# Kernel optimization log

Hardware: AMD Instinct MI355X
Metric: run time of the kernel (lower is better)

Reference implementation:

```python
import jax, jax.numpy as jnp
import numpy as np

N, T, E = 50000, 12, 800000
IN_DIM, SP_DIM, TP_DIM = 128, 128, 128


def setup_inputs() -> dict:
    key = jax.random.key(0)
    ks = jax.random.split(key, 9)
    h = jax.random.normal(ks[0], (N, T, IN_DIM), dtype=jnp.float32)
    src = jax.random.randint(ks[1], (E,), 0, N, dtype=jnp.int32)
    dst = jax.random.randint(ks[2], (E,), 0, N, dtype=jnp.int32)
    s = 1.0 / np.sqrt(IN_DIM).astype(np.float32)
    # GraphConv layer weights (xavier-ish) and zero biases, layer1: in->sp, layer2: sp->sp
    Wg1 = jax.random.normal(ks[3], (IN_DIM, SP_DIM), dtype=jnp.float32) * s
    bg1 = jnp.zeros((SP_DIM,), jnp.float32)
    Wg2 = jax.random.normal(ks[4], (SP_DIM, SP_DIM), dtype=jnp.float32) * s
    bg2 = jnp.zeros((SP_DIM,), jnp.float32)
    # LSTM params, torch layout: [4H, in]/[4H, H], gate order i,f,g,o
    t = 1.0 / np.sqrt(TP_DIM).astype(np.float32)
    w_ih = jax.random.uniform(ks[5], (4 * TP_DIM, IN_DIM), jnp.float32, -t, t)
    w_hh = jax.random.uniform(ks[6], (4 * TP_DIM, TP_DIM), jnp.float32, -t, t)
    b_ih = jax.random.uniform(ks[7], (4 * TP_DIM,), jnp.float32, -t, t)
    b_hh = jax.random.uniform(ks[8], (4 * TP_DIM,), jnp.float32, -t, t)
    return dict(h=h, src=src, dst=dst, Wg1=Wg1, bg1=bg1, Wg2=Wg2, bg2=bg2,
                w_ih=w_ih, w_hh=w_hh, b_ih=b_ih, b_hh=b_hh)


def _graph_conv(x, src, dst, norm_src, norm_dst, W, b):
    # DGL GraphConv norm='both': D_out^{-1/2} on source feats, sum-aggregate to dst,
    # D_in^{-1/2} on result, then dense weight + bias.
    x = x * norm_src                                  # [N, D]
    m = jax.ops.segment_sum(x[src], dst, num_segments=N)  # SpMM: [N, D]
    m = m * norm_dst
    return m @ W + b


def reference(h, src, dst, Wg1, bg1, Wg2, bg2, w_ih, w_hh, b_ih, b_hh):
    ones_e = jnp.ones((E,), jnp.float32)
    out_deg = jnp.maximum(jax.ops.segment_sum(ones_e, src, num_segments=N), 1.0)
    in_deg = jnp.maximum(jax.ops.segment_sum(ones_e, dst, num_segments=N), 1.0)
    norm_src = (out_deg ** -0.5)[:, None]
    norm_dst = (in_deg ** -0.5)[:, None]

    hs_list = []
    for i in range(T):  # fixed small time horizon
        x = h[:, i]  # [N, IN_DIM]
        x = jax.nn.gelu(_graph_conv(x, src, dst, norm_src, norm_dst, Wg1, bg1), approximate=False)
        x = jax.nn.gelu(_graph_conv(x, src, dst, norm_src, norm_dst, Wg2, bg2), approximate=False)
        hs_list.append(jnp.mean(x, axis=0))  # dgl.mean_nodes over the single graph
    hs = jnp.stack(hs_list, axis=0)[None]  # [1, T, SP_DIM]

    # temporal branch: LSTM over time, nodes as batch, then mean over time
    def lstm_step(carry, x_t):
        hp, cp = carry
        gates = x_t @ w_ih.T + b_ih + hp @ w_hh.T + b_hh  # [N, 4H]
        i_, f_, g_, o_ = jnp.split(gates, 4, axis=-1)
        c = jax.nn.sigmoid(f_) * cp + jax.nn.sigmoid(i_) * jnp.tanh(g_)
        ho = jax.nn.sigmoid(o_) * jnp.tanh(c)
        return (ho, c), ho

    h0 = jnp.zeros((N, TP_DIM), jnp.float32)
    _, ht_seq = jax.lax.scan(lstm_step, (h0, h0), jnp.swapaxes(h, 0, 1))  # [T, N, H]
    ht = jnp.mean(ht_seq, axis=0)  # torch.mean over dim=1 (time) -> [N, H]
    return hs, ht
```

## Files before the change

kernel.cpp:

```cpp
#include <hip/hip_runtime.h>
#include <math.h>

#define NN 50000
#define TT 12
#define EE 800000
#define DIM 128

typedef short bf16x8 __attribute__((ext_vector_type(8)));
typedef float f32x4 __attribute__((ext_vector_type(4)));

__device__ __forceinline__ float sigmoidf_(float x) { return 1.0f / (1.0f + expf(-x)); }
__device__ __forceinline__ float geluf_(float x) {
  return 0.5f * x * (1.0f + erff(x * 0.70710678118654752440f));
}
__device__ __forceinline__ unsigned short f2b(float f) {
  union { float f; unsigned u; } v;
  v.f = f;
  unsigned r = (v.u + 0x7fffu + ((v.u >> 16) & 1u)) >> 16;
  return (unsigned short)r;
}
__device__ __forceinline__ float blo(unsigned u) {
  union { unsigned x; float f; } v; v.x = u << 16; return v.f;
}
__device__ __forceinline__ float bhi(unsigned u) {
  union { unsigned x; float f; } v; v.x = u & 0xffff0000u; return v.f;
}
__device__ __forceinline__ float b2f(unsigned short b) {
  union { unsigned u; float f; } v; v.u = ((unsigned)b) << 16; return v.f;
}
__device__ __forceinline__ unsigned short f2h(float f) {
  union { _Float16 h; unsigned short s; } v; v.h = (_Float16)f; return v.s;
}
__device__ __forceinline__ float h2f(unsigned u) {
  union { unsigned short s; _Float16 h; } v; v.s = (unsigned short)u; return (float)v.h;
}


__global__ void deg_kernel(const int* __restrict__ src, const int* __restrict__ dst,
                           int* __restrict__ ds, int* __restrict__ dd) {
  int e = blockIdx.x * 256 + threadIdx.x;
  if (e < EE) {
    atomicAdd(&ds[src[e]], 1);
    atomicAdd(&dd[dst[e]], 1);
  }
}

__global__ void norm_kernel(const int* __restrict__ ds, const int* __restrict__ dd,
                            float* __restrict__ ns, float* __restrict__ nd) {
  int i = blockIdx.x * 256 + threadIdx.x;
  if (i < NN) {
    ns[i] = rsqrtf((float)(ds[i] > 1 ? ds[i] : 1));
    nd[i] = rsqrtf((float)(dd[i] > 1 ? dd[i] : 1));
  }
}

__global__ void scan_kernel(const int* __restrict__ cnt, int* __restrict__ row_ptr, int n) {
  __shared__ int sm[1024];
  __shared__ int carry;
  int tid = threadIdx.x;
  if (tid == 0) carry = 0;
  __syncthreads();
  for (int base = 0; base < n; base += 1024) {
    int v = (base + tid < n) ? cnt[base + tid] : 0;
    sm[tid] = v;
    __syncthreads();
    for (int off = 1; off < 1024; off <<= 1) {
      int t = (tid >= off) ? sm[tid - off] : 0;
      __syncthreads();
      sm[tid] += t;
      __syncthreads();
    }
    int incl = sm[tid];
    if (base + tid < n) row_ptr[base + tid] = carry + incl - v;
    int tot = sm[1023];
    __syncthreads();
    if (tid == 0) carry += tot;
    __syncthreads();
  }
  if (tid == 0) row_ptr[n] = carry;
}

__global__ void csr_kernel(const int* __restrict__ src, const int* __restrict__ dst,
                           const int* __restrict__ row_ptr, int* __restrict__ fill,
                           int* __restrict__ col) {
  int e = blockIdx.x * 256 + threadIdx.x;
  if (e < EE) {
    int d = dst[e];
    int pos = row_ptr[d] + atomicAdd(&fill[d], 1);
    col[pos] = src[e];
  }
}


__global__ void prep_w(const float* __restrict__ Wg1, const float* __restrict__ Wg2,
                       const float* __restrict__ wih, const float* __restrict__ whh,
                       const float* __restrict__ bih, const float* __restrict__ bhh,
                       unsigned short* __restrict__ W2bt, unsigned short* __restrict__ Wcomb,
                       unsigned short* __restrict__ whhb, float* __restrict__ bgate) {
  int i = blockIdx.x * 256 + threadIdx.x;
  if (i < 16384) {
    int n = i >> 7, k = i & 127;
    W2bt[i] = f2b(Wg2[k * 128 + n]);
  }
  int j = i - 16384;
  if (j >= 0 && j < 81920) {
    int n = j >> 7, k = j & 127;
    Wcomb[j] = f2b(n < 128 ? Wg1[k * 128 + n] : wih[(n - 128) * 128 + k]);
  }
  int q = i - (16384 + 81920);
  if (q >= 0 && q < 65536) whhb[q] = f2b(whh[q]);
  if (i < 512) bgate[i] = bih[i] + bhh[i];
}

#define LDT 40

__global__ __launch_bounds__(256) void gemm_h_fused(
    const float* __restrict__ A, const float* __restrict__ ns,
    const unsigned short* __restrict__ Wcomb, unsigned short* __restrict__ C,
    unsigned short* __restrict__ xg, int M) {
  __shared__ unsigned short As[128 * LDT];
  __shared__ unsigned short Bs[128 * LDT];
  const int cb = blockIdx.x;
  const unsigned short* Bt = Wcomb + cb * 16384;
  const int tid = threadIdx.x;
  const int lane = tid & 63, wid = tid >> 6;
  const int quad = lane >> 4, l16 = lane & 15;
  const int row0 = blockIdx.y * 128;
  const int wm = (wid >> 1) * 64, wn = (wid & 1) * 64;
  f32x4 acc[4][4] = {};
  for (int k0 = 0; k0 < 128; k0 += 32) {
#pragma unroll
    for (int rds = 0; rds < 2; rds++) {
      int idx = (rds * 256 + tid) * 8;
      int m = idx >> 5, c = idx & 31;
      int gr = row0 + m;
      if (gr >= M) gr = M - 1;
      const float4 va = *(const float4*)(A + (size_t)gr * 128 + k0 + c);
      const float4 vb = *(const float4*)(A + (size_t)gr * 128 + k0 + c + 4);
      unsigned short* d = &As[m * LDT + c];
      d[0] = f2b(va.x); d[1] = f2b(va.y); d[2] = f2b(va.z); d[3] = f2b(va.w);
      d[4] = f2b(vb.x); d[5] = f2b(vb.y); d[6] = f2b(vb.z); d[7] = f2b(vb.w);
      *(uint4*)(&Bs[m * LDT + c]) = *(const uint4*)(Bt + m * 128 + k0 + c);
    }
    __syncthreads();
    bf16x8 af[4], bfr[4];
#pragma unroll
    for (int im = 0; im < 4; im++)
      af[im] = *(const bf16x8*)(&As[(wm + im * 16 + l16) * LDT + quad * 8]);
#pragma unroll
    for (int in = 0; in < 4; in++)
      bfr[in] = *(const bf16x8*)(&Bs[(wn + in * 16 + l16) * LDT + quad * 8]);
#pragma unroll
    for (int im = 0; im < 4; im++)
#pragma unroll
      for (int in = 0; in < 4; in++)
        acc[im][in] = __builtin_amdgcn_mfma_f32_16x16x32_bf16(af[im], bfr[in], acc[im][in], 0, 0, 0);
    __syncthreads();
  }
  if (cb == 0) {
#pragma unroll
    for (int im = 0; im < 4; im++)
#pragma unroll
      for (int r = 0; r < 4; r++) {
        int row = row0 + wm + im * 16 + quad * 4 + r;
        if (row < M) {
          float s = ns[row / TT];
#pragma unroll
          for (int in = 0; in < 4; in++)
            C[(size_t)row * 128 + wn + in * 16 + l16] = f2b(acc[im][in][r] * s);
        }
      }
  } else {
    const int g = cb - 1;
#pragma unroll
    for (int im = 0; im < 4; im++)
#pragma unroll
      for (int r = 0; r < 4; r++) {
        int row = row0 + wm + im * 16 + quad * 4 + r;
        if (row < M)
#pragma unroll
          for (int in = 0; in < 4; in++) {
            int colc = wn + in * 16 + l16;
            xg[(size_t)row * 512 + colc * 4 + g] = f2h(acc[im][in][r]);
          }
      }
  }
}

__global__ __launch_bounds__(256) void gemm_bf16A(
    const unsigned short* __restrict__ A, const unsigned short* __restrict__ Bt,
    unsigned short* __restrict__ C, int M) {
  __shared__ unsigned short As[128 * LDT];
  __shared__ unsigned short Bs[128 * LDT];
  const int tid = threadIdx.x;
  const int lane = tid & 63, wid = tid >> 6;
  const int quad = lane >> 4, l16 = lane & 15;
  const int row0 = blockIdx.x * 128;
  const int wm = (wid >> 1) * 64, wn = (wid & 1) * 64;
  f32x4 acc[4][4] = {};
  for (int k0 = 0; k0 < 128; k0 += 32) {
#pragma unroll
    for (int rds = 0; rds < 2; rds++) {
      int idx = (rds * 256 + tid) * 8;
      int m = idx >> 5, c = idx & 31;
      int gr = row0 + m;
      if (gr >= M) gr = M - 1;
      *(uint4*)(&As[m * LDT + c]) = *(const uint4*)(A + (size_t)gr * 128 + k0 + c);
      *(uint4*)(&Bs[m * LDT + c]) = *(const uint4*)(Bt + m * 128 + k0 + c);
    }
    __syncthreads();
    bf16x8 af[4], bfr[4];
#pragma unroll
    for (int im = 0; im < 4; im++)
      af[im] = *(const bf16x8*)(&As[(wm + im * 16 + l16) * LDT + quad * 8]);
#pragma unroll
    for (int in = 0; in < 4; in++)
      bfr[in] = *(const bf16x8*)(&Bs[(wn + in * 16 + l16) * LDT + quad * 8]);
#pragma unroll
    for (int im = 0; im < 4; im++)
#pragma unroll
      for (int in = 0; in < 4; in++)
        acc[im][in] = __builtin_amdgcn_mfma_f32_16x16x32_bf16(af[im], bfr[in], acc[im][in], 0, 0, 0);
    __syncthreads();
  }
#pragma unroll
  for (int im = 0; im < 4; im++)
#pragma unroll
    for (int r = 0; r < 4; r++) {
      int row = row0 + wm + im * 16 + quad * 4 + r;
      if (row < M)
#pragma unroll
        for (int in = 0; in < 4; in++)
          C[(size_t)row * 128 + wn + in * 16 + l16] = f2b(acc[im][in][r]);
    }
}


template <bool SCALE_OUT>
__global__ __launch_bounds__(256) void spmm_b(
    const unsigned short* __restrict__ z, const int* __restrict__ rowp,
    const int* __restrict__ colx, const float* __restrict__ ns,
    const float* __restrict__ nd, const float* __restrict__ bg,
    unsigned short* __restrict__ y) {
  int d = (blockIdx.x * 256 + threadIdx.x) >> 6;
  int lane = threadIdx.x & 63;
  if (d >= NN) return;
  int beg = rowp[d], end = rowp[d + 1];
  float acc[3][8] = {};
  int j = beg;
  int s = (j < end) ? colx[j] : 0;
  while (j < end) {
    int snext = (j + 1 < end) ? colx[j + 1] : 0;
    const unsigned short* base = z + (size_t)s * 1536 + lane * 8;
#pragma unroll
    for (int r = 0; r < 3; r++) {
      uint4 v = *(const uint4*)(base + r * 512);
      acc[r][0] += blo(v.x); acc[r][1] += bhi(v.x);
      acc[r][2] += blo(v.y); acc[r][3] += bhi(v.y);
      acc[r][4] += blo(v.z); acc[r][5] += bhi(v.z);
      acc[r][6] += blo(v.w); acc[r][7] += bhi(v.w);
    }
    s = snext;
    j++;
  }
  float scn = nd[d];
  float sco = SCALE_OUT ? ns[d] : 1.0f;
  float bgv[8];
#pragma unroll
  for (int k = 0; k < 8; k++) bgv[k] = bg[(lane * 8 + k) & 127];
  unsigned short* outp = y + (size_t)d * 1536 + lane * 8;
#pragma unroll
  for (int r = 0; r < 3; r++) {
    unsigned short o[8];
#pragma unroll
    for (int k = 0; k < 8; k++)
      o[k] = f2b(sco * geluf_(acc[r][k] * scn + bgv[k]));
    *(uint4*)(outp + r * 512) = *(const uint4*)o;
  }
}


__global__ void colmean_b(const unsigned short* __restrict__ x, float* __restrict__ out) {
  int t = blockIdx.x;
  int cc = threadIdx.x & 127;
  int half = threadIdx.x >> 7;
  float s = 0.f;
  for (int n = blockIdx.y * 2 + half; n < NN; n += 64)
    s += b2f(x[((size_t)n * TT + t) * 128 + cc]);
  __shared__ float sm[256];
  sm[threadIdx.x] = s;
  __syncthreads();
  if (threadIdx.x < 128)
    atomicAdd(&out[t * 128 + cc], (sm[threadIdx.x] + sm[threadIdx.x + 128]) * (1.0f / NN));
}

#define HPLD 136
#define WLD 136

__global__ __launch_bounds__(512, 2) void lstm_hh(
    const unsigned short* __restrict__ whhb, const unsigned short* __restrict__ xg,
    const float* __restrict__ bgate, float* __restrict__ ht_out, int M) {
  __shared__ unsigned short Ws[512 * WLD];
  __shared__ unsigned short Hp[64 * HPLD];
  const int tid = threadIdx.x;
  const int lane = tid & 63;
  const int w = tid >> 6;
  const int quad = lane >> 4, l16 = lane & 15;
  const int row0 = blockIdx.x * 64;
  const int colg = w * 16 + l16;

#pragma unroll
  for (int it = 0; it < 16; it++) {
    int idx = it * 512 + tid;
    int n = idx >> 4, c = (idx & 15) * 8;
    *(uint4*)(&Ws[n * WLD + c]) = *(const uint4*)(whhb + n * 128 + c);
  }

  float cs[4][4], hacc[4][4];
#pragma unroll
  for (int im = 0; im < 4; im++)
#pragma unroll
    for (int r = 0; r < 4; r++) { cs[im][r] = 0.f; hacc[im][r] = 0.f; }

  const float bi = bgate[colg], bff = bgate[128 + colg];
  const float bgg = bgate[256 + colg], bo = bgate[384 + colg];
  __syncthreads();

  for (int t = 0; t < TT; t++) {
    uint2 xv[4][4];
#pragma unroll
    for (int im = 0; im < 4; im++)
#pragma unroll
      for (int r = 0; r < 4; r++) {
        int gr = row0 + im * 16 + quad * 4 + r;
        int grc = gr < M ? gr : M - 1;
        xv[im][r] = *(const uint2*)(xg + ((size_t)grc * TT + t) * 512 + colg * 4);
      }

    f32x4 acc[4][4] = {};
    if (t) {
#pragma unroll
      for (int k0 = 0; k0 < 128; k0 += 32) {
        bf16x8 af[4];
#pragma unroll
        for (int im = 0; im < 4; im++)
          af[im] = *(const bf16x8*)(&Hp[(im * 16 + l16) * HPLD + k0 + quad * 8]);
#pragma unroll
        for (int g = 0; g < 4; g++) {
          bf16x8 bf = *(const bf16x8*)(&Ws[(g * 128 + colg) * WLD + k0 + quad * 8]);
#pragma unroll
          for (int im = 0; im < 4; im++)
            acc[im][g] = __builtin_amdgcn_mfma_f32_16x16x32_bf16(af[im], bf, acc[im][g], 0, 0, 0);
        }
      }
      __syncthreads();
    }

#pragma unroll
    for (int im = 0; im < 4; im++)
#pragma unroll
      for (int r = 0; r < 4; r++) {
        float iv = sigmoidf_(acc[im][0][r] + h2f(xv[im][r].x & 0xffffu) + bi);
        float fv = sigmoidf_(acc[im][1][r] + h2f(xv[im][r].x >> 16) + bff);
        float gv = tanhf(acc[im][2][r] + h2f(xv[im][r].y & 0xffffu) + bgg);
        float ov = sigmoidf_(acc[im][3][r] + h2f(xv[im][r].y >> 16) + bo);
        float cn = fv * cs[im][r] + iv * gv;
        cs[im][r] = cn;
        float ho = ov * tanhf(cn);
        hacc[im][r] += ho;
        Hp[(im * 16 + quad * 4 + r) * HPLD + colg] = f2b(ho);
      }
    __syncthreads();
  }
#pragma unroll
  for (int im = 0; im < 4; im++)
#pragma unroll
    for (int r = 0; r < 4; r++) {
      int gr = row0 + im * 16 + quad * 4 + r;
      if (gr < M) ht_out[(size_t)gr * 128 + colg] = hacc[im][r] * (1.0f / TT);
    }
}


extern "C" void kernel_launch(void* const* d_in, const int* in_sizes, int n_in,
                              void* d_out, int out_size, void* d_ws, size_t ws_size,
                              hipStream_t stream) {
  const float* h   = (const float*)d_in[0];
  const int*   src = (const int*)d_in[1];
  const int*   dst = (const int*)d_in[2];
  const float* Wg1 = (const float*)d_in[3];
  const float* bg1 = (const float*)d_in[4];
  const float* Wg2 = (const float*)d_in[5];
  const float* bg2 = (const float*)d_in[6];
  const float* wih = (const float*)d_in[7];
  const float* whh = (const float*)d_in[8];
  const float* bih = (const float*)d_in[9];
  const float* bhh = (const float*)d_in[10];

  float* out = (float*)d_out;
  float* hs_out = out;
  float* ht_out = out + TT * DIM;

  char* p = (char*)d_ws;
  auto alloc = [&](size_t bytes) -> void* {
    void* r = (void*)p;
    p += (bytes + 255) & ~(size_t)255;
    return r;
  };
  const size_t MB = (size_t)NN * TT * DIM;
  unsigned short* bufA = (unsigned short*)alloc(MB * 2);
  unsigned short* bufB = (unsigned short*)alloc(MB * 2);
  unsigned short* xgb  = (unsigned short*)alloc((size_t)NN * TT * 512 * 2);
  unsigned short* W2bt = (unsigned short*)alloc(16384 * 2);
  unsigned short* Wcomb= (unsigned short*)alloc(81920 * 2);
  unsigned short* whhb = (unsigned short*)alloc(65536 * 2);
  float* bgate = (float*)alloc(512 * 4);
  float* ns    = (float*)alloc(NN * 4);
  float* nd    = (float*)alloc(NN * 4);
  int* degs    = (int*)alloc(NN * 4);
  int* degd    = (int*)alloc(NN * 4);
  int* rowp    = (int*)alloc((NN + 1) * 4);
  int* colx    = (int*)alloc(EE * 4);

  hipMemsetAsync(degs, 0, NN * 4, stream);
  hipMemsetAsync(degd, 0, NN * 4, stream);
  hipMemsetAsync(hs_out, 0, TT * DIM * 4, stream);

  deg_kernel<<<(EE + 255) / 256, 256, 0, stream>>>(src, dst, degs, degd);
  norm_kernel<<<(NN + 255) / 256, 256, 0, stream>>>(degs, degd, ns, nd);
  scan_kernel<<<1, 1024, 0, stream>>>(degd, rowp, NN);
  hipMemsetAsync(degs, 0, NN * 4, stream);
  csr_kernel<<<(EE + 255) / 256, 256, 0, stream>>>(src, dst, rowp, degs, colx);
  prep_w<<<(16384 + 81920 + 65536 + 255) / 256, 256, 0, stream>>>(
      Wg1, Wg2, wih, whh, bih, bhh, W2bt, Wcomb, whhb, bgate);

  const int M = NN * TT;
  const int gblocks = (M + 127) / 128;
  const int sblocks = (NN + 3) / 4;

  gemm_h_fused<<<dim3(5, gblocks), 256, 0, stream>>>(h, ns, Wcomb, bufA, xgb, M);
  spmm_b<true><<<sblocks, 256, 0, stream>>>(bufA, rowp, colx, ns, nd, bg1, bufB);
  gemm_bf16A<<<gblocks, 256, 0, stream>>>(bufB, W2bt, bufA, M);
  spmm_b<false><<<sblocks, 256, 0, stream>>>(bufA, rowp, colx, ns, nd, bg2, bufB);
  colmean_b<<<dim3(TT, 32), 256, 0, stream>>>(bufB, hs_out);

  lstm_hh<<<(NN + 63) / 64, 512, 0, stream>>>(whhb, xgb, bgate, ht_out, NN);
}
```

Before: 2.881 ms.

## Load each h row tile once and loop over all five weight column blocks

The input GEMM now runs one block per 128-row tile. That block converts the fp32 h tile to bf16 in shared memory once, then loops over the five 128-column weight blocks (Wg1 plus the four LSTM gates), so h is no longer re-read five times. The xg gate-input layout changes from interleaved [col][gate] to gate-major [gate][col], giving coalesced 16-bit stores, and the LSTM kernel now does four strided scalar loads instead of one 8-byte load. Shared memory per block grows, which may lower occupancy, and the grid shrinks fivefold.

```diff
diff --git a/kernel.cpp b/kernel.cpp
--- a/kernel.cpp
+++ b/kernel.cpp
@@ -31,8 +31,8 @@
 __device__ __forceinline__ unsigned short f2h(float f) {
   union { _Float16 h; unsigned short s; } v; v.h = (_Float16)f; return v.s;
 }
-__device__ __forceinline__ float h2f(unsigned u) {
-  union { unsigned short s; _Float16 h; } v; v.s = (unsigned short)u; return (float)v.h;
+__device__ __forceinline__ float h2f(unsigned short u) {
+  union { unsigned short s; _Float16 h; } v; v.s = u; return (float)v.h;
 }
 
 
@@ -114,76 +114,85 @@
 
 #define LDT 40
 
-__global__ __launch_bounds__(256) void gemm_h_fused(
+__global__ __launch_bounds__(256) void gemm_h_all(
     const float* __restrict__ A, const float* __restrict__ ns,
     const unsigned short* __restrict__ Wcomb, unsigned short* __restrict__ C,
     unsigned short* __restrict__ xg, int M) {
-  __shared__ unsigned short As[128 * LDT];
+  __shared__ unsigned short As[4 * 128 * LDT];
   __shared__ unsigned short Bs[128 * LDT];
-  const int cb = blockIdx.x;
-  const unsigned short* Bt = Wcomb + cb * 16384;
   const int tid = threadIdx.x;
   const int lane = tid & 63, wid = tid >> 6;
   const int quad = lane >> 4, l16 = lane & 15;
-  const int row0 = blockIdx.y * 128;
+  const int row0 = blockIdx.x * 128;
   const int wm = (wid >> 1) * 64, wn = (wid & 1) * 64;
-  f32x4 acc[4][4] = {};
-  for (int k0 = 0; k0 < 128; k0 += 32) {
-#pragma unroll
-    for (int rds = 0; rds < 2; rds++) {
-      int idx = (rds * 256 + tid) * 8;
-      int m = idx >> 5, c = idx & 31;
-      int gr = row0 + m;
-      if (gr >= M) gr = M - 1;
-      const float4 va = *(const float4*)(A + (size_t)gr * 128 + k0 + c);
-      const float4 vb = *(const float4*)(A + (size_t)gr * 128 + k0 + c + 4);
-      unsigned short* d = &As[m * LDT + c];
-      d[0] = f2b(va.x); d[1] = f2b(va.y); d[2] = f2b(va.z); d[3] = f2b(va.w);
-      d[4] = f2b(vb.x); d[5] = f2b(vb.y); d[6] = f2b(vb.z); d[7] = f2b(vb.w);
-      *(uint4*)(&Bs[m * LDT + c]) = *(const uint4*)(Bt + m * 128 + k0 + c);
-    }
-    __syncthreads();
-    bf16x8 af[4], bfr[4];
-#pragma unroll
-    for (int im = 0; im < 4; im++)
-      af[im] = *(const bf16x8*)(&As[(wm + im * 16 + l16) * LDT + quad * 8]);
-#pragma unroll
-    for (int in = 0; in < 4; in++)
-      bfr[in] = *(const bf16x8*)(&Bs[(wn + in * 16 + l16) * LDT + quad * 8]);
-#pragma unroll
-    for (int im = 0; im < 4; im++)
+
+#pragma unroll
+  for (int rds = 0; rds < 8; rds++) {
+    int idx = rds * 256 + tid;
+    int m = idx >> 4;
+    int k8 = (idx & 15) * 8;
+    int gr = row0 + m;
+    if (gr >= M) gr = M - 1;
+    const float4 va = *(const float4*)(A + (size_t)gr * 128 + k8);
+    const float4 vb = *(const float4*)(A + (size_t)gr * 128 + k8 + 4);
+    int chunk = k8 >> 5, c = k8 & 31;
+    unsigned short* d = &As[(chunk * 128 + m) * LDT + c];
+    d[0] = f2b(va.x); d[1] = f2b(va.y); d[2] = f2b(va.z); d[3] = f2b(va.w);
+    d[4] = f2b(vb.x); d[5] = f2b(vb.y); d[6] = f2b(vb.z); d[7] = f2b(vb.w);
+  }
+
+  for (int cb = 0; cb < 5; cb++) {
+    f32x4 acc[4][4] = {};
+#pragma unroll
+    for (int k0 = 0; k0 < 4; k0++) {
+      __syncthreads();
+      {
+        int n = tid >> 1;
+        int c = (tid & 1) * 16;
+        const unsigned short* srcw = Wcomb + ((size_t)(cb * 128 + n)) * 128 + k0 * 32 + c;
+        *(uint4*)(&Bs[n * LDT + c]) = *(const uint4*)srcw;
+        *(uint4*)(&Bs[n * LDT + c + 8]) = *(const uint4*)(srcw + 8);
+      }
+      __syncthreads();
+      bf16x8 af[4], bfr[4];
+#pragma unroll
+      for (int im = 0; im < 4; im++)
+        af[im] = *(const bf16x8*)(&As[(k0 * 128 + wm + im * 16 + l16) * LDT + quad * 8]);
 #pragma unroll
       for (int in = 0; in < 4; in++)
-        acc[im][in] = __builtin_amdgcn_mfma_f32_16x16x32_bf16(af[im], bfr[in], acc[im][in], 0, 0, 0);
-    __syncthreads();
-  }
-  if (cb == 0) {
-#pragma unroll
-    for (int im = 0; im < 4; im++)
-#pragma unroll
-      for (int r = 0; r < 4; r++) {
-        int row = row0 + wm + im * 16 + quad * 4 + r;
-        if (row < M) {
-          float s = ns[row / TT];
-#pragma unroll
-          for (int in = 0; in < 4; in++)
-            C[(size_t)row * 128 + wn + in * 16 + l16] = f2b(acc[im][in][r] * s);
+        bfr[in] = *(const bf16x8*)(&Bs[(wn + in * 16 + l16) * LDT + quad * 8]);
+#pragma unroll
+      for (int im = 0; im < 4; im++)
+#pragma unroll
+        for (int in = 0; in < 4; in++)
+          acc[im][in] = __builtin_amdgcn_mfma_f32_16x16x32_bf16(af[im], bfr[in], acc[im][in], 0, 0, 0);
+    }
+    if (cb == 0) {
+#pragma unroll
+      for (int im = 0; im < 4; im++)
+#pragma unroll
+        for (int r = 0; r < 4; r++) {
+          int row = row0 + wm + im * 16 + quad * 4 + r;
+          if (row < M) {
+            float s = ns[row / TT];
+#pragma unroll
+            for (int in = 0; in < 4; in++)
+              C[(size_t)row * 128 + wn + in * 16 + l16] = f2b(acc[im][in][r] * s);
+          }
         }
-      }
-  } else {
-    const int g = cb - 1;
-#pragma unroll
-    for (int im = 0; im < 4; im++)
-#pragma unroll
-      for (int r = 0; r < 4; r++) {
-        int row = row0 + wm + im * 16 + quad * 4 + r;
-        if (row < M)
-#pragma unroll
-          for (int in = 0; in < 4; in++) {
-            int colc = wn + in * 16 + l16;
-            xg[(size_t)row * 512 + colc * 4 + g] = f2h(acc[im][in][r]);
-          }
-      }
+    } else {
+      const int goff = (cb - 1) * 128;
+#pragma unroll
+      for (int im = 0; im < 4; im++)
+#pragma unroll
+        for (int r = 0; r < 4; r++) {
+          int row = row0 + wm + im * 16 + quad * 4 + r;
+          if (row < M)
+#pragma unroll
+            for (int in = 0; in < 4; in++)
+              xg[(size_t)row * 512 + goff + wn + in * 16 + l16] = f2h(acc[im][in][r]);
+        }
+    }
   }
 }
 
@@ -327,14 +336,16 @@
   __syncthreads();
 
   for (int t = 0; t < TT; t++) {
-    uint2 xv[4][4];
+    unsigned short xsv[4][4][4];
 #pragma unroll
     for (int im = 0; im < 4; im++)
 #pragma unroll
       for (int r = 0; r < 4; r++) {
         int gr = row0 + im * 16 + quad * 4 + r;
         int grc = gr < M ? gr : M - 1;
-        xv[im][r] = *(const uint2*)(xg + ((size_t)grc * TT + t) * 512 + colg * 4);
+        const unsigned short* xp = xg + ((size_t)grc * TT + t) * 512 + colg;
+#pragma unroll
+        for (int g = 0; g < 4; g++) xsv[im][r][g] = xp[g * 128];
       }
 
     f32x4 acc[4][4] = {};
@@ -360,10 +371,10 @@
     for (int im = 0; im < 4; im++)
 #pragma unroll
       for (int r = 0; r < 4; r++) {
-        float iv = sigmoidf_(acc[im][0][r] + h2f(xv[im][r].x & 0xffffu) + bi);
-        float fv = sigmoidf_(acc[im][1][r] + h2f(xv[im][r].x >> 16) + bff);
-        float gv = tanhf(acc[im][2][r] + h2f(xv[im][r].y & 0xffffu) + bgg);
-        float ov = sigmoidf_(acc[im][3][r] + h2f(xv[im][r].y >> 16) + bo);
+        float iv = sigmoidf_(acc[im][0][r] + h2f(xsv[im][r][0]) + bi);
+        float fv = sigmoidf_(acc[im][1][r] + h2f(xsv[im][r][1]) + bff);
+        float gv = tanhf(acc[im][2][r] + h2f(xsv[im][r][2]) + bgg);
+        float ov = sigmoidf_(acc[im][3][r] + h2f(xsv[im][r][3]) + bo);
         float cn = fv * cs[im][r] + iv * gv;
         cs[im][r] = cn;
         float ho = ov * tanhf(cn);
@@ -438,7 +449,7 @@
   const int gblocks = (M + 127) / 128;
   const int sblocks = (NN + 3) / 4;
 
-  gemm_h_fused<<<dim3(5, gblocks), 256, 0, stream>>>(h, ns, Wcomb, bufA, xgb, M);
+  gemm_h_all<<<gblocks, 256, 0, stream>>>(h, ns, Wcomb, bufA, xgb, M);
   spmm_b<true><<<sblocks, 256, 0, stream>>>(bufA, rowp, colx, ns, nd, bg1, bufB);
   gemm_bf16A<<<gblocks, 256, 0, stream>>>(bufB, W2bt, bufA, M);
   spmm_b<false><<<sblocks, 256, 0, stream>>>(bufA, rowp, colx, ns, nd, bg2, bufB);
```

Measured after the change: 2.442 ms. 1.18x faster.
